# Kernel tuning notes

Measured on AMD Instinct MI355X. Metric: run time of the kernel, lower is better.

## Reference

```python
import jax, jax.numpy as jnp
import numpy as np

EMBED_DIM = 1024
NUM_HEADS = 16
HEAD_DIM = EMBED_DIM // NUM_HEADS


def setup_inputs() -> dict:
    key = jax.random.key(0)
    ks = jax.random.split(key, 11)
    B, T, C = 2, 2048, EMBED_DIM
    s = 1.0 / np.sqrt(C)  # ~ torch Linear init scale
    inp = {
        "q": jax.random.normal(ks[0], (B, T, C), jnp.float32),
        "k": jax.random.normal(ks[1], (B, T, C), jnp.float32),
        "v": jax.random.normal(ks[2], (B, T, C), jnp.float32),
        "Wq": jax.random.normal(ks[3], (C, C), jnp.float32) * s,
        "bq": jax.random.normal(ks[4], (C,), jnp.float32) * s,
        "Wk": jax.random.normal(ks[5], (C, C), jnp.float32) * s,
        "bk": jax.random.normal(ks[6], (C,), jnp.float32) * s,
        "Wv": jax.random.normal(ks[7], (C, C), jnp.float32) * s,
        "bv": jax.random.normal(ks[8], (C,), jnp.float32) * s,
        "Wo": jax.random.normal(ks[9], (C, C), jnp.float32) * s,
        "bo": jax.random.normal(ks[10], (C,), jnp.float32) * s,
    }
    return inp


def _split_heads(x):
    B, T, C = x.shape
    return x.reshape(B, T, NUM_HEADS, HEAD_DIM).transpose(0, 2, 1, 3)  # [B,H,T,Dh]


def reference(q, k, v, Wq, bq, Wk, bk, Wv, bv, Wo, bo):
    B, Tq, C = q.shape
    # torch Linear: y = x @ W.T + b
    qh = _split_heads(q @ Wq.T + bq)
    kh = _split_heads(k @ Wk.T + bk)
    vh = _split_heads(v @ Wv.T + bv)
    scale = 1.0 / np.sqrt(HEAD_DIM).astype(np.float32)
    logits = jnp.einsum("bhqd,bhkd->bhqk", qh, kh) * scale
    attn = jax.nn.softmax(logits, axis=-1)
    out = jnp.einsum("bhqk,bhkd->bhqd", attn, vh)
    out = out.transpose(0, 2, 1, 3).reshape(B, Tq, C)
    return out @ Wo.T + bo
```

## Files before the change

kernel.cpp:

```cpp
#include <hip/hip_runtime.h>
#include <stdint.h>

#define T_SEQ 2048
#define CDIM 1024
#define NHEAD 16
#define HDIM 64
#define MROWS 4096

typedef unsigned short u16;
typedef __attribute__((ext_vector_type(8))) short bf16x8;
typedef __attribute__((ext_vector_type(4))) float f32x4;
typedef __attribute__((ext_vector_type(16))) float f32x16;
typedef __attribute__((ext_vector_type(4))) unsigned short u16x4;
typedef __attribute__((ext_vector_type(4))) unsigned int uint4v;

#if __has_builtin(__builtin_amdgcn_exp2f)
#define EXP2(x) __builtin_amdgcn_exp2f(x)
#else
#define EXP2(x) exp2f(x)
#endif

__device__ __forceinline__ u16 f2bf(float f) {
  unsigned u = __builtin_bit_cast(unsigned, f);
  u += 0x7fffu + ((u >> 16) & 1u);
  return (u16)(u >> 16);
}

__device__ __forceinline__ float bf2f(unsigned hw) {
  return __builtin_bit_cast(float, hw << 16);
}

__device__ __forceinline__ unsigned cvt_pk_bf16(float lo, float hi) {
  unsigned r;
  asm("v_cvt_pk_bf16_f32 %0, %1, %2" : "=v"(r) : "v"(lo), "v"(hi));
  return r;
}

__device__ __forceinline__ void pls(unsigned &a, unsigned &b) {
  asm("v_permlane32_swap_b32 %0, %1" : "+v"(a), "+v"(b));
}

__device__ __forceinline__ void gll16(const void* g, void* l) {
  __builtin_amdgcn_global_load_lds((__attribute__((address_space(1))) void*)(g),
                                   (__attribute__((address_space(3))) void*)(l),
                                   16, 0, 0);
}

__device__ __forceinline__ void wg_barrier() {
  asm volatile("" ::: "memory");
  __builtin_amdgcn_s_barrier();
  asm volatile("" ::: "memory");
}

#define WAIT_VM(N) do { __builtin_amdgcn_s_waitcnt(0xF00 | 0x70 | (N)); \
                        asm volatile("" ::: "memory"); } while (0)

__device__ __forceinline__ int xcd_lid(int wgid, int cpx) {
  return (wgid & 7) * cpx + (wgid >> 3);
}

__global__ __launch_bounds__(256)
void cvt_all(const float* __restrict__ q, const float* __restrict__ k, const float* __restrict__ v,
             const float* __restrict__ wq, const float* __restrict__ wk,
             const float* __restrict__ wv, const float* __restrict__ wo,
             u16* __restrict__ qb, u16* __restrict__ kb, u16* __restrict__ vb,
             u16* __restrict__ wqb, u16* __restrict__ wkb, u16* __restrict__ wvb, u16* __restrict__ wob) {
  int b = blockIdx.x;
  const float* src; u16* dst; int base;
  if (b < 1536) {
    int s = b >> 9;
    src = (s == 0) ? q : (s == 1) ? k : v;
    dst = (s == 0) ? qb : (s == 1) ? kb : vb;
    base = (b & 511) * 2048;
  } else {
    int s = (b - 1536) >> 7;
    src = (s == 0) ? wq : (s == 1) ? wk : (s == 2) ? wv : wo;
    dst = (s == 0) ? wqb : (s == 1) ? wkb : (s == 2) ? wvb : wob;
    base = ((b - 1536) & 127) * 2048;
  }
#pragma unroll
  for (int j = 0; j < 8; ++j) {
    int i = base + j * 256 + threadIdx.x;
    float4 a = ((const float4*)src)[i];
    u16x4 o = { f2bf(a.x), f2bf(a.y), f2bf(a.z), f2bf(a.w) };
    ((u16x4*)dst)[i] = o;
  }
}


__device__ __forceinline__ void gemm_stage(const u16* Ag, const u16* Bg, u16* Ad, u16* Bd) {
#pragma unroll
  for (int c = 0; c < 4; ++c) {
    gll16(Ag + c * 32 * CDIM, Ad + c * 2048);
    gll16(Bg + c * 32 * CDIM, Bd + c * 2048);
  }
}

__device__ __forceinline__ void gemm_compute(const u16* As, const u16* Bs,
                                             f32x4 (&acc)[4][4],
                                             int wr, int wc, int lg, int lr) {
#pragma unroll
  for (int kk = 0; kk < 2; ++kk) {
    bf16x8 af[4], bfr[4];
#pragma unroll
    for (int f = 0; f < 4; ++f) {
      int ra = wr * 64 + f * 16 + lr;
      af[f]  = *(const bf16x8*)((const char*)As + ra * 128 + ((lg * 16 + kk * 64) ^ ((ra & 7) << 4)));
      int rb = wc * 64 + f * 16 + lr;
      bfr[f] = *(const bf16x8*)((const char*)Bs + rb * 128 + ((lg * 16 + kk * 64) ^ ((rb & 7) << 4)));
    }
#pragma unroll
    for (int i = 0; i < 4; ++i)
#pragma unroll
      for (int j = 0; j < 4; ++j)
        acc[i][j] = __builtin_amdgcn_mfma_f32_16x16x32_bf16(af[i], bfr[j], acc[i][j], 0, 0, 0);
  }
}

#define GEMM_KLOOP_SB(Asb, Bsb, Ad, Bd)                                        \
  _Pragma("unroll 1")                                                          \
  for (int kt = 0; kt < 16; ++kt) {                                            \
    __syncthreads();                                                           \
    gemm_stage(Ag + kt * 64, Bg + kt * 64, Ad, Bd);                            \
    __syncthreads();                                                           \
    gemm_compute(Asb, Bsb, acc, wr, wc, lg, lr);                               \
  }

__global__ __launch_bounds__(256)
void gemm_qkv(const u16* __restrict__ A0, const u16* __restrict__ A1, const u16* __restrict__ A2,
              const u16* __restrict__ W0, const u16* __restrict__ W1, const u16* __restrict__ W2,
              const float* __restrict__ b0, const float* __restrict__ b1, const float* __restrict__ b2,
              u16* __restrict__ o0, u16* __restrict__ o1, u16* __restrict__ o2,
              float qscale) {
  __shared__ u16 Asb[128 * 64];
  __shared__ u16 Bsb[128 * 64];
  int wgid = blockIdx.x + 8 * (blockIdx.y + 32 * blockIdx.z);
  int lid = xcd_lid(wgid, 96);
  const int bx = lid & 7, by = (lid >> 3) & 31, z = lid >> 8;

  const u16* A   = (z == 0) ? A0 : (z == 1) ? A1 : A2;
  const u16* Bw  = (z == 0) ? W0 : (z == 1) ? W1 : W2;
  const float* bias = (z == 0) ? b0 : (z == 1) ? b1 : b2;
  u16* outp = (z == 0) ? o0 : (z == 1) ? o1 : o2;
  const float scale = (z == 0) ? qscale : 1.0f;

  const int m0 = by * 128;
  const int n0 = bx * 128;
  const int tid = threadIdx.x;
  const int w = tid >> 6, l = tid & 63;
  const int wr = w >> 1, wc = w & 1;
  const int lg = l >> 4, lr = l & 15;

  const int row0 = tid >> 3, slot0 = tid & 7;
  const int so = (slot0 ^ (row0 & 7)) << 3;
  const u16* Ag = A  + ((size_t)(m0 + row0)) * CDIM + so;
  const u16* Bg = Bw + ((size_t)(n0 + row0)) * CDIM + so;
  u16* Ad = Asb + w * 512;
  u16* Bd = Bsb + w * 512;

  f32x4 acc[4][4] = {};

  GEMM_KLOOP_SB(Asb, Bsb, Ad, Bd)

#pragma unroll
  for (int fj = 0; fj < 4; ++fj) {
    int col = n0 + wc * 64 + fj * 16 + lr;
    float bv = bias[col];
    int h = col >> 6, d = col & 63;
#pragma unroll
    for (int fi = 0; fi < 4; ++fi) {
#pragma unroll
      for (int i = 0; i < 4; ++i) {
        int row = m0 + wr * 64 + fi * 16 + lg * 4 + i;
        float val = (acc[fi][fj][i] + bv) * scale;
        int b = row >> 11, t = row & 2047;
        if (z < 2)
          outp[(((size_t)(b * NHEAD + h)) * T_SEQ + t) * HDIM + d] = f2bf(val);
        else
          outp[(((size_t)(b * NHEAD + h)) * HDIM + d) * T_SEQ + t] = f2bf(val);
      }
    }
  }
}

__global__ __launch_bounds__(256)
void gemm_bt0(const u16* __restrict__ A, const u16* __restrict__ Bw,
              const float* __restrict__ bias, float* __restrict__ outp) {
  __shared__ u16 Asb[128 * 64];
  __shared__ u16 Bsb[128 * 64];
  int wgid = blockIdx.x + 8 * blockIdx.y;
  int lid = xcd_lid(wgid, 32);
  const int bx = lid & 7, by = lid >> 3;

  const int m0 = by * 128;
  const int n0 = bx * 128;
  const int tid = threadIdx.x;
  const int w = tid >> 6, l = tid & 63;
  const int wr = w >> 1, wc = w & 1;
  const int lg = l >> 4, lr = l & 15;

  const int row0 = tid >> 3, slot0 = tid & 7;
  const int so = (slot0 ^ (row0 & 7)) << 3;
  const u16* Ag = A  + ((size_t)(m0 + row0)) * CDIM + so;
  const u16* Bg = Bw + ((size_t)(n0 + row0)) * CDIM + so;
  u16* Ad = Asb + w * 512;
  u16* Bd = Bsb + w * 512;

  f32x4 acc[4][4] = {};

  GEMM_KLOOP_SB(Asb, Bsb, Ad, Bd)

#pragma unroll
  for (int fj = 0; fj < 4; ++fj) {
    int col = n0 + wc * 64 + fj * 16 + lr;
    float bv = bias[col];
#pragma unroll
    for (int fi = 0; fi < 4; ++fi) {
#pragma unroll
      for (int i = 0; i < 4; ++i) {
        int row = m0 + wr * 64 + fi * 16 + lg * 4 + i;
        outp[(size_t)row * CDIM + col] = acc[fi][fj][i] + bv;
      }
    }
  }
}


__device__ __forceinline__ void attn_tile(const char* Kb, const char* Vb,
                                          const bf16x8 (&qf)[4],
                                          f32x16 (&acc)[2], f32x4& lsum, float& m_run,
                                          int lo5, int hi, int swz) {
  f32x16 s[2] = {};
  const int colK = 16 * hi;
  __builtin_amdgcn_s_setprio(1);
#pragma unroll
  for (int st = 0; st < 4; ++st) {
    bf16x8 k0 = *(const bf16x8*)(Kb + lo5 * 128        + ((32 * st + colK) ^ swz));
    bf16x8 k1 = *(const bf16x8*)(Kb + (lo5 + 32) * 128 + ((32 * st + colK) ^ swz));
    s[0] = __builtin_amdgcn_mfma_f32_32x32x16_bf16(k0, qf[st], s[0], 0, 0, 0);
    s[1] = __builtin_amdgcn_mfma_f32_32x32x16_bf16(k1, qf[st], s[1], 0, 0, 0);
  }
  __builtin_amdgcn_s_setprio(0);

  float t[8];
#pragma unroll
  for (int i = 0; i < 8; ++i)
    t[i] = fmaxf(fmaxf(s[0][2 * i], s[0][2 * i + 1]), fmaxf(s[1][2 * i], s[1][2 * i + 1]));
  float u0 = fmaxf(fmaxf(t[0], t[1]), fmaxf(t[2], t[3]));
  float u1 = fmaxf(fmaxf(t[4], t[5]), fmaxf(t[6], t[7]));
  float tl = fmaxf(u0, u1);
  if (!__all(tl <= m_run + 8.f)) {
    float tmax = fmaxf(tl, __shfl_xor(tl, 32));
    float m_new = fmaxf(m_run, tmax);
    float alpha = EXP2(m_run - m_new);
    lsum[0] *= alpha; lsum[1] *= alpha; lsum[2] *= alpha; lsum[3] *= alpha;
#pragma unroll
    for (int i = 0; i < 16; ++i) { acc[0][i] *= alpha; acc[1][i] *= alpha; }
    m_run = m_new;
  }

  unsigned pg[2][8];
#pragma unroll
  for (int g = 0; g < 8; ++g) {
    float a0 = EXP2(s[0][2 * g] - m_run), b0 = EXP2(s[0][2 * g + 1] - m_run);
    float a1 = EXP2(s[1][2 * g] - m_run), b1 = EXP2(s[1][2 * g + 1] - m_run);
    lsum[g & 3] += (a0 + b0) + (a1 + b1);
    pg[0][g] = cvt_pk_bf16(a0, b0);
    pg[1][g] = cvt_pk_bf16(a1, b1);
  }

  bf16x8 pb[4];
#pragma unroll
  for (int sub = 0; sub < 2; ++sub)
#pragma unroll
    for (int ks = 0; ks < 2; ++ks) {
      unsigned w0 = pg[sub][4 * ks + 0], w1 = pg[sub][4 * ks + 1];
      unsigned w2 = pg[sub][4 * ks + 2], w3 = pg[sub][4 * ks + 3];
      pls(w0, w2); pls(w1, w3);
      uint4v tt = { w0, w1, w2, w3 };
      pb[2 * sub + ks] = __builtin_bit_cast(bf16x8, tt);
    }

  __builtin_amdgcn_s_setprio(1);
#pragma unroll
  for (int ks = 0; ks < 4; ++ks) {
    bf16x8 v0 = *(const bf16x8*)(Vb + lo5 * 128        + ((32 * ks + colK) ^ swz));
    bf16x8 v1 = *(const bf16x8*)(Vb + (lo5 + 32) * 128 + ((32 * ks + colK) ^ swz));
    acc[0] = __builtin_amdgcn_mfma_f32_32x32x16_bf16(v0, pb[ks], acc[0], 0, 0, 0);
    acc[1] = __builtin_amdgcn_mfma_f32_32x32x16_bf16(v1, pb[ks], acc[1], 0, 0, 0);
  }
  __builtin_amdgcn_s_setprio(0);
}

__global__ __launch_bounds__(512, 4)
void attn_fused(const u16* __restrict__ Qh, const u16* __restrict__ Kh,
                const u16* __restrict__ Vt, u16* __restrict__ Op,
                float2* __restrict__ ml) {
  __shared__ u16 S[5 * 8192];
  int wgid = blockIdx.x + 8 * (blockIdx.y + 32 * blockIdx.z);
  int lid = xcd_lid(wgid, 64);
  const int bqx = lid & 7, bh = (lid >> 3) & 31, half = lid >> 8;
  const int q0 = bqx * 256;
  const int tid = threadIdx.x;
  const int w = tid >> 6, l = tid & 63;
  const int lo5 = l & 31, hi = l >> 5;
  const int swz = (l & 7) << 4;

  const u16* qptr = Qh + ((size_t)bh * T_SEQ + q0 + w * 32 + lo5) * HDIM + hi * 8;
  bf16x8 qf[4];
#pragma unroll
  for (int s = 0; s < 4; ++s) qf[s] = *(const bf16x8*)(qptr + 16 * s);

  const int isV = w >> 2;
  const int rbase = (w & 3) * 16;
  const int srow = rbase + (l >> 3);
  const int soff = ((l & 7) ^ ((l >> 3) & 7)) << 3;
  const u16* Kgs = Kh + ((size_t)bh * T_SEQ + srow) * HDIM + soff;
  const u16* Vgs = Vt + ((size_t)bh * HDIM + srow) * T_SEQ + soff;

  auto stage = [&](int t, int slot) {
    if (!isV) {
      u16* dst = S + slot * 8192 + rbase * 64;
      const u16* src = Kgs + (size_t)t * 64 * HDIM;
      gll16(src, dst);
      gll16(src + 8 * HDIM, dst + 8 * 64);
    } else {
      u16* dst = S + slot * 8192 + 4096 + rbase * 64;
      const u16* src = Vgs + t * 64;
      gll16(src, dst);
      gll16(src + (size_t)8 * T_SEQ, dst + 8 * 64);
    }
  };

  f32x16 acc[2] = {};
  f32x4 lsum = {};
  float m_run = -1e30f;
  const int tb = half * 16;

  stage(tb + 0, 0);
  stage(tb + 1, 1);
  stage(tb + 2, 2);
  int cs = 0, ps = 3;
#pragma unroll 1
  for (int s = 0; s < 16; ++s) {
    int ns = (s + 3 < 16) ? s + 3 : 15;
    stage(tb + ns, ps);
    WAIT_VM(6);
    wg_barrier();
    attn_tile((const char*)(S + cs * 8192), (const char*)(S + cs * 8192 + 4096),
              qf, acc, lsum, m_run, lo5, hi, swz);
    cs = (cs == 4) ? 0 : cs + 1;
    ps = (ps == 4) ? 0 : ps + 1;
  }

  float ls = (lsum[0] + lsum[1]) + (lsum[2] + lsum[3]);
  ls += __shfl_xor(ls, 32);
  float inv = 1.f / ls;

  WAIT_VM(0);
  wg_barrier();
  char* os = (char*)&S[0] + w * 4096;
#pragma unroll
  for (int dsub = 0; dsub < 2; ++dsub)
#pragma unroll
    for (int gg = 0; gg < 4; ++gg) {
      unsigned wa = cvt_pk_bf16(acc[dsub][4 * gg + 0] * inv, acc[dsub][4 * gg + 1] * inv);
      unsigned wb = cvt_pk_bf16(acc[dsub][4 * gg + 2] * inv, acc[dsub][4 * gg + 3] * inv);
      uint2 wv = { wa, wb };
      int byte = lo5 * 128 + (((32 * dsub + 8 * gg + 4 * hi) * 2) ^ swz);
      *(uint2*)(os + byte) = wv;
    }
  u16* orow = Op + ((size_t)(half * 32 + bh) * T_SEQ + q0 + w * 32) * HDIM;
#pragma unroll
  for (int c = 0; c < 4; ++c) {
    int qq = 8 * c + (l >> 3);
    uint4v ov = *(const uint4v*)(os + qq * 128 + ((16 * (l & 7)) ^ ((qq & 7) << 4)));
    *(uint4v*)(orow + qq * HDIM + (l & 7) * 8) = ov;
  }
  if (hi == 0)
    ml[(size_t)(half * 32 + bh) * T_SEQ + q0 + w * 32 + lo5] = make_float2(m_run, ls);
}

__global__ __launch_bounds__(256)
void attn_combine(const u16* __restrict__ Op, const float2* __restrict__ ml,
                  u16* __restrict__ Ao) {
  int task0 = blockIdx.x * 256 + threadIdx.x;
#pragma unroll 1
  for (int it = 0; it < 4; ++it) {
    int task = task0 + it * 131072;
    int chunk = task & 7;
    int q  = (task >> 3) & 2047;
    int bh = task >> 14;
    float2 ml0 = ml[(size_t)bh * T_SEQ + q];
    float2 ml1 = ml[(size_t)(32 + bh) * T_SEQ + q];
    float M = fmaxf(ml0.x, ml1.x);
    float w0 = EXP2(ml0.x - M) * ml0.y;
    float w1 = EXP2(ml1.x - M) * ml1.y;
    float zi = 1.f / (w0 + w1);
    float a0 = w0 * zi, a1 = w1 * zi;
    const u16* p0 = Op + ((size_t)bh * T_SEQ + q) * HDIM + chunk * 8;
    const u16* p1 = Op + ((size_t)(32 + bh) * T_SEQ + q) * HDIM + chunk * 8;
    uint4v o0 = *(const uint4v*)p0;
    uint4v o1 = *(const uint4v*)p1;
    uint4v ov;
#pragma unroll
    for (int j = 0; j < 4; ++j) {
      float lo = a0 * bf2f(o0[j] & 0xffffu)  + a1 * bf2f(o1[j] & 0xffffu);
      float hi = a0 * bf2f(o0[j] >> 16)      + a1 * bf2f(o1[j] >> 16);
      ov[j] = cvt_pk_bf16(lo, hi);
    }
    int b = bh >> 4, h = bh & 15;
    *(uint4v*)(Ao + ((size_t)(b * T_SEQ + q)) * CDIM + h * HDIM + chunk * 8) = ov;
  }
}

extern "C" void kernel_launch(void* const* d_in, const int* in_sizes, int n_in,
                              void* d_out, int out_size, void* d_ws, size_t ws_size,
                              hipStream_t stream) {
  const float* q  = (const float*)d_in[0];
  const float* k  = (const float*)d_in[1];
  const float* v  = (const float*)d_in[2];
  const float* Wq = (const float*)d_in[3];
  const float* bq = (const float*)d_in[4];
  const float* Wk = (const float*)d_in[5];
  const float* bk = (const float*)d_in[6];
  const float* Wv = (const float*)d_in[7];
  const float* bv = (const float*)d_in[8];
  const float* Wo = (const float*)d_in[9];
  const float* bo = (const float*)d_in[10];

  char* ws = (char*)d_ws;
  size_t off = 0;
  auto alloc = [&](size_t n) { void* p = ws + off; off += (n + 255) & ~(size_t)255; return p; };
  const size_t NX = (size_t)MROWS * CDIM;
  const size_t NW = (size_t)CDIM * CDIM;
  u16* qb  = (u16*)alloc(NX * 2);
  u16* kb  = (u16*)alloc(NX * 2);
  u16* vb  = (u16*)alloc(NX * 2);
  u16* Wqb = (u16*)alloc(NW * 2);
  u16* Wkb = (u16*)alloc(NW * 2);
  u16* Wvb = (u16*)alloc(NW * 2);
  u16* Wob = (u16*)alloc(NW * 2);
  u16* Qhp = (u16*)alloc(NX * 2);
  u16* Khp = (u16*)alloc(NX * 2);
  u16* Vtp = (u16*)alloc(NX * 2);
  u16* Aop = (u16*)alloc(NX * 2);

  u16* Op = qb;
  float2* mlp = (float2*)vb;

  cvt_all<<<2048, 256, 0, stream>>>(q, k, v, Wq, Wk, Wv, Wo,
                                    qb, kb, vb, Wqb, Wkb, Wvb, Wob);

  const float qscale = 0.18033688011112042f;
  gemm_qkv<<<dim3(CDIM / 128, MROWS / 128, 3), 256, 0, stream>>>(
      qb, kb, vb, Wqb, Wkb, Wvb, bq, bk, bv, Qhp, Khp, Vtp, qscale);

  attn_fused<<<dim3(T_SEQ / 256, 32, 2), 512, 0, stream>>>(Qhp, Khp, Vtp, Op, mlp);
  attn_combine<<<512, 256, 0, stream>>>(Op, mlp, Aop);

  gemm_bt0<<<dim3(CDIM / 128, MROWS / 128), 256, 0, stream>>>(Aop, Wob, bo, (float*)d_out);

  (void)in_sizes; (void)n_in; (void)out_size; (void)ws_size;
}
```

Baseline: 138.5 us.

## Fuse fp32-to-bf16 activation conversion into QKV GEMM operand loading

The QKV projection GEMM now reads fp32 q/k/v straight from global memory, converts them to bf16 in registers and writes them to shared memory, instead of relying on a separate conversion kernel. The conversion kernel now handles only the weights. This removes a full write and re-read of the bf16 activation copies. In exchange, the A-operand load becomes synchronous register loads plus LDS stores rather than async direct-to-LDS loads, and each GEMM tile re-reads fp32 data, which is twice as many bytes. Op and mlp buffers now get dedicated workspace allocations.

```diff
diff --git a/kernel.cpp b/kernel.cpp
--- a/kernel.cpp
+++ b/kernel.cpp
@@ -60,24 +60,15 @@
 }
 
 __global__ __launch_bounds__(256)
-void cvt_all(const float* __restrict__ q, const float* __restrict__ k, const float* __restrict__ v,
-             const float* __restrict__ wq, const float* __restrict__ wk,
-             const float* __restrict__ wv, const float* __restrict__ wo,
-             u16* __restrict__ qb, u16* __restrict__ kb, u16* __restrict__ vb,
-             u16* __restrict__ wqb, u16* __restrict__ wkb, u16* __restrict__ wvb, u16* __restrict__ wob) {
+void cvt_w(const float* __restrict__ wq, const float* __restrict__ wk,
+           const float* __restrict__ wv, const float* __restrict__ wo,
+           u16* __restrict__ wqb, u16* __restrict__ wkb,
+           u16* __restrict__ wvb, u16* __restrict__ wob) {
   int b = blockIdx.x;
-  const float* src; u16* dst; int base;
-  if (b < 1536) {
-    int s = b >> 9;
-    src = (s == 0) ? q : (s == 1) ? k : v;
-    dst = (s == 0) ? qb : (s == 1) ? kb : vb;
-    base = (b & 511) * 2048;
-  } else {
-    int s = (b - 1536) >> 7;
-    src = (s == 0) ? wq : (s == 1) ? wk : (s == 2) ? wv : wo;
-    dst = (s == 0) ? wqb : (s == 1) ? wkb : (s == 2) ? wvb : wob;
-    base = ((b - 1536) & 127) * 2048;
-  }
+  int s = b >> 7;
+  const float* src = (s == 0) ? wq : (s == 1) ? wk : (s == 2) ? wv : wo;
+  u16* dst = (s == 0) ? wqb : (s == 1) ? wkb : (s == 2) ? wvb : wob;
+  int base = (b & 127) * 2048;
 #pragma unroll
   for (int j = 0; j < 8; ++j) {
     int i = base + j * 256 + threadIdx.x;
@@ -127,7 +118,7 @@
   }
 
 __global__ __launch_bounds__(256)
-void gemm_qkv(const u16* __restrict__ A0, const u16* __restrict__ A1, const u16* __restrict__ A2,
+void gemm_qkv(const float* __restrict__ A0, const float* __restrict__ A1, const float* __restrict__ A2,
               const u16* __restrict__ W0, const u16* __restrict__ W1, const u16* __restrict__ W2,
               const float* __restrict__ b0, const float* __restrict__ b1, const float* __restrict__ b2,
               u16* __restrict__ o0, u16* __restrict__ o1, u16* __restrict__ o2,
@@ -138,8 +129,8 @@
   int lid = xcd_lid(wgid, 96);
   const int bx = lid & 7, by = (lid >> 3) & 31, z = lid >> 8;
 
-  const u16* A   = (z == 0) ? A0 : (z == 1) ? A1 : A2;
-  const u16* Bw  = (z == 0) ? W0 : (z == 1) ? W1 : W2;
+  const float* A  = (z == 0) ? A0 : (z == 1) ? A1 : A2;
+  const u16* Bw   = (z == 0) ? W0 : (z == 1) ? W1 : W2;
   const float* bias = (z == 0) ? b0 : (z == 1) ? b1 : b2;
   u16* outp = (z == 0) ? o0 : (z == 1) ? o1 : o2;
   const float scale = (z == 0) ? qscale : 1.0f;
@@ -153,14 +144,30 @@
 
   const int row0 = tid >> 3, slot0 = tid & 7;
   const int so = (slot0 ^ (row0 & 7)) << 3;
-  const u16* Ag = A  + ((size_t)(m0 + row0)) * CDIM + so;
-  const u16* Bg = Bw + ((size_t)(n0 + row0)) * CDIM + so;
-  u16* Ad = Asb + w * 512;
+  const float* Agf = A + ((size_t)(m0 + row0)) * CDIM + so;
+  const u16*   Bg  = Bw + ((size_t)(n0 + row0)) * CDIM + so;
   u16* Bd = Bsb + w * 512;
 
   f32x4 acc[4][4] = {};
 
-  GEMM_KLOOP_SB(Asb, Bsb, Ad, Bd)
+#pragma unroll 1
+  for (int kt = 0; kt < 16; ++kt) {
+    __syncthreads();
+#pragma unroll
+    for (int c = 0; c < 4; ++c)
+      gll16(Bg + kt * 64 + c * 32 * CDIM, Bd + c * 2048);
+#pragma unroll
+    for (int c = 0; c < 4; ++c) {
+      const float* ap = Agf + kt * 64 + (size_t)c * 32 * CDIM;
+      float4 fa = ((const float4*)ap)[0];
+      float4 fb = ((const float4*)ap)[1];
+      uint4v pk = { cvt_pk_bf16(fa.x, fa.y), cvt_pk_bf16(fa.z, fa.w),
+                    cvt_pk_bf16(fb.x, fb.y), cvt_pk_bf16(fb.z, fb.w) };
+      *(uint4v*)(Asb + (size_t)(c * 256 + tid) * 8) = pk;
+    }
+    __syncthreads();
+    gemm_compute(Asb, Bsb, acc, wr, wc, lg, lr);
+  }
 
 #pragma unroll
   for (int fj = 0; fj < 4; ++fj) {
@@ -434,9 +441,6 @@
   auto alloc = [&](size_t n) { void* p = ws + off; off += (n + 255) & ~(size_t)255; return p; };
   const size_t NX = (size_t)MROWS * CDIM;
   const size_t NW = (size_t)CDIM * CDIM;
-  u16* qb  = (u16*)alloc(NX * 2);
-  u16* kb  = (u16*)alloc(NX * 2);
-  u16* vb  = (u16*)alloc(NX * 2);
   u16* Wqb = (u16*)alloc(NW * 2);
   u16* Wkb = (u16*)alloc(NW * 2);
   u16* Wvb = (u16*)alloc(NW * 2);
@@ -445,16 +449,14 @@
   u16* Khp = (u16*)alloc(NX * 2);
   u16* Vtp = (u16*)alloc(NX * 2);
   u16* Aop = (u16*)alloc(NX * 2);
-
-  u16* Op = qb;
-  float2* mlp = (float2*)vb;
-
-  cvt_all<<<2048, 256, 0, stream>>>(q, k, v, Wq, Wk, Wv, Wo,
-                                    qb, kb, vb, Wqb, Wkb, Wvb, Wob);
+  u16* Op  = (u16*)alloc(NX * 2 * 2);
+  float2* mlp = (float2*)alloc((size_t)64 * T_SEQ * sizeof(float2));
+
+  cvt_w<<<512, 256, 0, stream>>>(Wq, Wk, Wv, Wo, Wqb, Wkb, Wvb, Wob);
 
   const float qscale = 0.18033688011112042f;
   gemm_qkv<<<dim3(CDIM / 128, MROWS / 128, 3), 256, 0, stream>>>(
-      qb, kb, vb, Wqb, Wkb, Wvb, bq, bk, bv, Qhp, Khp, Vtp, qscale);
+      q, k, v, Wqb, Wkb, Wvb, bq, bk, bv, Qhp, Khp, Vtp, qscale);
 
   attn_fused<<<dim3(T_SEQ / 256, 32, 2), 512, 0, stream>>>(Qhp, Khp, Vtp, Op, mlp);
   attn_combine<<<512, 256, 0, stream>>>(Op, mlp, Aop);
```

Result: no change. 136.3 us (-1.6%).
